# Optimization experiments

Hardware: AMD Instinct MI355X
Metric: run time of the kernel (lower is better)

Reference implementation:

```python
import jax, jax.numpy as jnp
import numpy as np

B, N, D_MODEL, HIDDEN, ACTION_BIN = 4096, 8, 1024, 2048, 256


def setup_inputs() -> dict:
    key = jax.random.key(0)
    k_x, k_w1, k_b1, k_w2, k_b2 = jax.random.split(key, 5)
    # per-action-dim MLP weights stacked along leading n axis
    s1 = 1.0 / np.sqrt(D_MODEL)
    s2 = 1.0 / np.sqrt(HIDDEN)
    return {
        "x": jax.random.normal(k_x, (B, N, D_MODEL), dtype=jnp.float32),
        "W1": jax.random.normal(k_w1, (N, D_MODEL, HIDDEN), dtype=jnp.float32) * s1,
        "b1": jax.random.normal(k_b1, (N, HIDDEN), dtype=jnp.float32) * s1,
        "W2": jax.random.normal(k_w2, (N, HIDDEN, ACTION_BIN), dtype=jnp.float32) * s2,
        "b2": jax.random.normal(k_b2, (N, ACTION_BIN), dtype=jnp.float32) * s2,
    }


def reference(x, W1, b1, W2, b2):
    # Original torch module loops over n slices, each with its own
    # Linear(d_model->hidden) -> ReLU -> Linear(hidden->action_bin).
    # Equivalent grouped/batched matmul over the n axis:
    x = x.astype(jnp.float32)
    h = jnp.einsum('bnd,ndh->bnh', x, W1) + b1[None, :, :]   # [b, n, hidden]
    h = jax.nn.relu(h)
    out = jnp.einsum('bnh,nha->bna', h, W2) + b2[None, :, :]  # [b, n, action_bin]
    return out
```

## Files before the change

### kernel.cpp

```cpp
#include <hip/hip_runtime.h>
#include <stdint.h>

#define BTOT   4096
#define NGRP   8
#define DMODEL 1024
#define HIDDEN 2048
#define ABIN   256

typedef short bf16x8 __attribute__((ext_vector_type(8)));
typedef float f32x4  __attribute__((ext_vector_type(4)));

__device__ __forceinline__ ushort f2bf(float f) {
    union { float f; uint32_t u; } v; v.f = f;
    return (ushort)((v.u + 0x7FFFu + ((v.u >> 16) & 1u)) >> 16);
}

__device__ __forceinline__ void gl_lds16(const ushort* g, ushort* l) {
    __builtin_amdgcn_global_load_lds(
        (const __attribute__((address_space(1))) uint32_t*)g,
        (__attribute__((address_space(3))) uint32_t*)l,
        16, 0, 0);
}

__global__ void transpose_w(const float* __restrict__ W, ushort* __restrict__ Wt,
                            int K, int N)
{
    __shared__ float tl[32][33];
    const int n  = blockIdx.y;
    const int nt = blockIdx.x % (N / 32);
    const int kt = blockIdx.x / (N / 32);
    const float* Wn  = W  + (size_t)n * K * N;
    ushort*      Wtn = Wt + (size_t)n * N * K;
    const int tx = threadIdx.x & 31, ty = threadIdx.x >> 5;
#pragma unroll
    for (int j = 0; j < 4; j++)
        tl[ty + 8 * j][tx] = Wn[(size_t)(kt * 32 + ty + 8 * j) * N + nt * 32 + tx];
    __syncthreads();
#pragma unroll
    for (int j = 0; j < 4; j++) {
        const int r = ty + 8 * j;
        Wtn[(size_t)(nt * 32 + r) * K + kt * 32 + tx] = f2bf(tl[tx][r]);
    }
}

__global__ void conv_x(const float* __restrict__ x, ushort* __restrict__ xb,
                       int CH, int cb)
{
    const int flat = blockIdx.x * 256 + threadIdx.x;
    const int d8 = flat & 127;
    const int rem = flat >> 7;
    const int n = rem & 7;
    const int r = rem >> 3;
    const float* src = x + ((size_t)(cb + r) * NGRP + n) * DMODEL + d8 * 8;
    float4 v0 = *(const float4*)(src);
    float4 v1 = *(const float4*)(src + 4);
    bf16x8 p;
    p[0] = (short)f2bf(v0.x); p[1] = (short)f2bf(v0.y);
    p[2] = (short)f2bf(v0.z); p[3] = (short)f2bf(v0.w);
    p[4] = (short)f2bf(v1.x); p[5] = (short)f2bf(v1.y);
    p[6] = (short)f2bf(v1.z); p[7] = (short)f2bf(v1.w);
    *(bf16x8*)(xb + ((size_t)n * CH + r) * DMODEL + d8 * 8) = p;
}

template<int MODE>
__global__ __launch_bounds__(256, 2)
void gemm_bt(const ushort* __restrict__ A, const ushort* __restrict__ Bt,
             const float* __restrict__ bias, void* __restrict__ outp,
             int CH, int cb)
{
    constexpr int K    = (MODE == 0) ? DMODEL : HIDDEN;
    constexpr int NDIM = (MODE == 0) ? HIDDEN : ABIN;
    constexpr int NT   = NDIM / 128;
    constexpr int BK   = 64;

    __shared__ __align__(16) ushort As[128 * BK];
    __shared__ __align__(16) ushort Bs[128 * BK];

    const int n  = blockIdx.y;
    const int mt = blockIdx.x / NT;
    const int nt = blockIdx.x % NT;

    const ushort* Ab = A  + ((size_t)n * CH   + mt * 128) * K;
    const ushort* Bb = Bt + ((size_t)n * NDIM + nt * 128) * K;

    const int t = threadIdx.x, l = t & 63, w = t >> 6;
    const int wr = w >> 1, wc = w & 1;
    const int lq = l >> 4, lr = l & 15;

    f32x4 acc[4][4];
#pragma unroll
    for (int i = 0; i < 4; i++)
#pragma unroll
        for (int j = 0; j < 4; j++) acc[i][j] = (f32x4){0.f, 0.f, 0.f, 0.f};

    for (int ki = 0; ki < K / BK; ++ki) {
        const ushort* Ak = Ab + ki * BK;
        const ushort* Bk = Bb + ki * BK;
        __syncthreads();
#pragma unroll
        for (int i = 0; i < 4; i++) {
            const int flat = t + 256 * i;
            const int row = flat >> 3, seg = flat & 7;
            gl_lds16(Ak + (size_t)row * K + seg * 8, (ushort*)As + flat * 8);
            gl_lds16(Bk + (size_t)row * K + seg * 8, (ushort*)Bs + flat * 8);
        }
        __syncthreads();

#pragma unroll
        for (int kk = 0; kk < 2; kk++) {
            bf16x8 af[4], bf[4];
#pragma unroll
            for (int m = 0; m < 4; m++)
                af[m] = *(const bf16x8*)&As[(wr * 64 + m * 16 + lr) * BK + kk * 32 + lq * 8];
#pragma unroll
            for (int nf = 0; nf < 4; nf++)
                bf[nf] = *(const bf16x8*)&Bs[(wc * 64 + nf * 16 + lr) * BK + kk * 32 + lq * 8];
#pragma unroll
            for (int m = 0; m < 4; m++)
#pragma unroll
                for (int nf = 0; nf < 4; nf++)
                    acc[m][nf] = __builtin_amdgcn_mfma_f32_16x16x32_bf16(af[m], bf[nf], acc[m][nf], 0, 0, 0);
        }
    }

#pragma unroll
    for (int nf = 0; nf < 4; nf++) {
        const int colg = nt * 128 + wc * 64 + nf * 16 + lr;
        const float bv = bias[(size_t)n * NDIM + colg];
#pragma unroll
        for (int m = 0; m < 4; m++) {
#pragma unroll
            for (int r = 0; r < 4; r++) {
                float vv = acc[m][nf][r] + bv;
                const int row = mt * 128 + wr * 64 + m * 16 + lq * 4 + r;
                if constexpr (MODE == 0) {
                    vv = fmaxf(vv, 0.f);
                    ((ushort*)outp)[((size_t)n * CH + row) * HIDDEN + colg] = f2bf(vv);
                } else {
                    ((float*)outp)[((size_t)(cb + row) * NGRP + n) * ABIN + colg] = vv;
                }
            }
        }
    }
}

extern "C" void kernel_launch(void* const* d_in, const int* in_sizes, int n_in,
                              void* d_out, int out_size, void* d_ws, size_t ws_size,
                              hipStream_t stream)
{
    const float* x  = (const float*)d_in[0];
    const float* W1 = (const float*)d_in[1];
    const float* b1 = (const float*)d_in[2];
    const float* W2 = (const float*)d_in[3];
    const float* b2 = (const float*)d_in[4];

    ushort* W1t = (ushort*)d_ws;
    ushort* W2t = W1t + (size_t)NGRP * HIDDEN * DMODEL;
    ushort* xb  = W2t + (size_t)NGRP * ABIN * HIDDEN;
    const size_t fixed = ((size_t)NGRP * HIDDEN * DMODEL + (size_t)NGRP * ABIN * HIDDEN) * 2;

    int CH = 4096;
    while (CH > 128 && fixed + (size_t)CH * (NGRP * (DMODEL + HIDDEN) * 2) > ws_size) CH >>= 1;
    ushort* h = xb + (size_t)NGRP * CH * DMODEL;

    {
        dim3 g1((DMODEL / 32) * (HIDDEN / 32), NGRP);
        transpose_w<<<g1, 256, 0, stream>>>(W1, W1t, DMODEL, HIDDEN);
        dim3 g2((HIDDEN / 32) * (ABIN / 32), NGRP);
        transpose_w<<<g2, 256, 0, stream>>>(W2, W2t, HIDDEN, ABIN);
    }

    for (int cb = 0; cb < BTOT; cb += CH) {
        conv_x<<<CH * 4, 256, 0, stream>>>(x, xb, CH, cb);
        dim3 g1((CH / 128) * (HIDDEN / 128), NGRP);
        gemm_bt<0><<<g1, 256, 0, stream>>>(xb, W1t, b1, h, CH, cb);
        dim3 g2((CH / 128) * (ABIN / 128), NGRP);
        gemm_bt<1><<<g2, 256, 0, stream>>>(h, W2t, b2, (float*)d_out, CH, cb);
    }
}
```

Baseline: 288.8 us.

## Replace first GEMM with 256x256-tile, 8-wave, double-buffered pipelined kernel

The first GEMM (x·W1 + bias + ReLU), which dominates the FLOPs, now runs in a dedicated kernel with 256x256 output tiles and 512 threads. It double-buffers 128KB of dynamic LDS, prefetching the next K-slab while MFMAs run on the current one. It adds an XOR-swizzled LDS layout to cut bank conflicts, a block-id swizzle for L2 locality, and s_setprio and sched_barrier hints around the MFMA bursts. The aim is to hide global-load latency and raise data reuse per tile, at the cost of heavy LDS use (one block per CU) and many explicit barriers and waitcnt steps.

```diff
diff --git a/kernel.cpp b/kernel.cpp
--- a/kernel.cpp
+++ b/kernel.cpp
@@ -62,17 +62,155 @@
     *(bf16x8*)(xb + ((size_t)n * CH + r) * DMODEL + d8 * 8) = p;
 }
 
-template<int MODE>
+#define REGN(buf,op,half,ks) (sm + ((((buf)*2+(op))*2+(half))*2+(ks))*4096)
+
+template<int MH>
+__device__ __forceinline__ void mma_q(f32x4 (&acc)[8][4], const bf16x8 (&af)[4],
+                                      const bf16x8 (&bv)[4])
+{
+#pragma unroll
+    for (int m4 = 0; m4 < 4; ++m4)
+#pragma unroll
+        for (int nf = 0; nf < 4; ++nf)
+            acc[MH * 4 + m4][nf] = __builtin_amdgcn_mfma_f32_16x16x32_bf16(
+                af[m4], bv[nf], acc[MH * 4 + m4][nf], 0, 0, 0);
+}
+
+__global__ __launch_bounds__(512, 2)
+void gemm8_1(const ushort* __restrict__ A, const ushort* __restrict__ Bt,
+             const float* __restrict__ bias, ushort* __restrict__ h, int CH)
+{
+    constexpr int K = DMODEL, NDIM = HIDDEN, KT = K / 64;
+    const int MT = CH >> 8, NT = NDIM >> 8;
+    extern __shared__ ushort sm[];
+
+    const int nwg = gridDim.x;
+    const int bid = blockIdx.x;
+    const int swz = (bid & 7) * (nwg >> 3) + (bid >> 3);
+    const int n   = swz / (MT * NT);
+    const int rem = swz - n * (MT * NT);
+    const int mt  = rem / NT;
+    const int nt  = rem - mt * NT;
+
+    const int tid = threadIdx.x;
+    const int l = tid & 63, wid = tid >> 6;
+    const int wr = wid >> 2, wc = wid & 3, wc2 = wc >> 1;
+    const int lq = l >> 4, lr = l & 15;
+
+    const ushort* Ab = A  + ((size_t)n * CH   + (size_t)mt * 256) * K;
+    const ushort* Bb = Bt + ((size_t)n * NDIM + (size_t)nt * 256) * K;
+
+    const int srow = tid >> 2;
+    const int sseg = (tid & 3) ^ (srow & 3);
+
+    auto stageA = [&](int b, int T, int ks) {
+        const size_t kofs = (size_t)T * 64 + ks * 32 + sseg * 8;
+        gl_lds16(Ab + (size_t)srow * K + kofs,         REGN(b, 0, 0, ks) + tid * 8);
+        gl_lds16(Ab + (size_t)(128 + srow) * K + kofs, REGN(b, 0, 1, ks) + tid * 8);
+    };
+    auto stageB = [&](int b, int T, int ks) {
+        const size_t kofs = (size_t)T * 64 + ks * 32 + sseg * 8;
+        gl_lds16(Bb + (size_t)srow * K + kofs,         REGN(b, 1, 0, ks) + tid * 8);
+        gl_lds16(Bb + (size_t)(128 + srow) * K + kofs, REGN(b, 1, 1, ks) + tid * 8);
+    };
+    auto ldA = [&](bf16x8 (&af)[4], int b, int kk, int mh) {
+#pragma unroll
+        for (int m4 = 0; m4 < 4; ++m4) {
+            const int rh = mh * 64 + m4 * 16 + lr;
+            af[m4] = *(const bf16x8*)(REGN(b, 0, wr, kk) + rh * 32 + (lq ^ (rh & 3)) * 8);
+        }
+    };
+    auto ldB = [&](bf16x8 (&bv)[4], int b, int kk) {
+#pragma unroll
+        for (int nf = 0; nf < 4; ++nf) {
+            const int rb = (wc & 1) * 64 + nf * 16 + lr;
+            bv[nf] = *(const bf16x8*)(REGN(b, 1, wc2, kk) + rb * 32 + (lq ^ (rb & 3)) * 8);
+        }
+    };
+
+    f32x4 acc[8][4];
+#pragma unroll
+    for (int i = 0; i < 8; ++i)
+#pragma unroll
+        for (int j = 0; j < 4; ++j) acc[i][j] = (f32x4){0.f, 0.f, 0.f, 0.f};
+
+    stageA(0, 0, 0); stageB(0, 0, 0); stageA(0, 0, 1); stageB(0, 0, 1);
+    asm volatile("s_waitcnt vmcnt(4)" ::: "memory");
+    __builtin_amdgcn_s_barrier();
+
+    bf16x8 af[4], bv[4];
+    for (int g = 0; g < KT; ++g) {
+        const int c = g & 1;
+        const bool ns = (g + 1 < KT);
+
+        ldA(af, c, 0, 0); ldB(bv, c, 0);
+        if (ns) stageA(c ^ 1, g + 1, 0);
+        __builtin_amdgcn_s_barrier();
+        asm volatile("s_waitcnt lgkmcnt(0)" ::: "memory");
+        __builtin_amdgcn_sched_barrier(0);
+        __builtin_amdgcn_s_setprio(1);
+        mma_q<0>(acc, af, bv);
+        __builtin_amdgcn_s_setprio(0);
+        __builtin_amdgcn_s_barrier();
+
+        ldA(af, c, 0, 1);
+        if (ns) stageB(c ^ 1, g + 1, 0);
+        __builtin_amdgcn_s_barrier();
+        asm volatile("s_waitcnt lgkmcnt(0)" ::: "memory");
+        __builtin_amdgcn_sched_barrier(0);
+        __builtin_amdgcn_s_setprio(1);
+        mma_q<1>(acc, af, bv);
+        __builtin_amdgcn_s_setprio(0);
+        if (ns) asm volatile("s_waitcnt vmcnt(4)" ::: "memory");
+        else    asm volatile("s_waitcnt vmcnt(0)" ::: "memory");
+        __builtin_amdgcn_s_barrier();
+
+        ldA(af, c, 1, 0); ldB(bv, c, 1);
+        if (ns) stageA(c ^ 1, g + 1, 1);
+        __builtin_amdgcn_s_barrier();
+        asm volatile("s_waitcnt lgkmcnt(0)" ::: "memory");
+        __builtin_amdgcn_sched_barrier(0);
+        __builtin_amdgcn_s_setprio(1);
+        mma_q<0>(acc, af, bv);
+        __builtin_amdgcn_s_setprio(0);
+        __builtin_amdgcn_s_barrier();
+
+        ldA(af, c, 1, 1);
+        if (ns) stageB(c ^ 1, g + 1, 1);
+        __builtin_amdgcn_s_barrier();
+        asm volatile("s_waitcnt lgkmcnt(0)" ::: "memory");
+        __builtin_amdgcn_sched_barrier(0);
+        __builtin_amdgcn_s_setprio(1);
+        mma_q<1>(acc, af, bv);
+        __builtin_amdgcn_s_setprio(0);
+        if (ns) asm volatile("s_waitcnt vmcnt(4)" ::: "memory");
+        __builtin_amdgcn_s_barrier();
+    }
+
+    __builtin_amdgcn_sched_barrier(0);
+
+#pragma unroll
+    for (int nf = 0; nf < 4; ++nf) {
+        const int col = nt * 256 + wc * 64 + nf * 16 + lr;
+        const float bvv = bias[(size_t)n * NDIM + col];
+#pragma unroll
+        for (int m = 0; m < 8; ++m) {
+#pragma unroll
+            for (int r = 0; r < 4; ++r) {
+                const int row = mt * 256 + wr * 128 + m * 16 + lq * 4 + r;
+                float vv = fmaxf(acc[m][nf][r] + bvv, 0.f);
+                h[((size_t)n * CH + row) * HIDDEN + col] = f2bf(vv);
+            }
+        }
+    }
+}
+
 __global__ __launch_bounds__(256, 2)
-void gemm_bt(const ushort* __restrict__ A, const ushort* __restrict__ Bt,
-             const float* __restrict__ bias, void* __restrict__ outp,
-             int CH, int cb)
-{
-    constexpr int K    = (MODE == 0) ? DMODEL : HIDDEN;
-    constexpr int NDIM = (MODE == 0) ? HIDDEN : ABIN;
-    constexpr int NT   = NDIM / 128;
-    constexpr int BK   = 64;
-
+void gemm2(const ushort* __restrict__ A, const ushort* __restrict__ Bt,
+           const float* __restrict__ bias, float* __restrict__ outp,
+           int CH, int cb)
+{
+    constexpr int K = HIDDEN, NDIM = ABIN, NT = NDIM / 128, BK = 64;
     __shared__ __align__(16) ushort As[128 * BK];
     __shared__ __align__(16) ushort Bs[128 * BK];
 
@@ -131,14 +269,8 @@
         for (int m = 0; m < 4; m++) {
 #pragma unroll
             for (int r = 0; r < 4; r++) {
-                float vv = acc[m][nf][r] + bv;
                 const int row = mt * 128 + wr * 64 + m * 16 + lq * 4 + r;
-                if constexpr (MODE == 0) {
-                    vv = fmaxf(vv, 0.f);
-                    ((ushort*)outp)[((size_t)n * CH + row) * HIDDEN + colg] = f2bf(vv);
-                } else {
-                    ((float*)outp)[((size_t)(cb + row) * NGRP + n) * ABIN + colg] = vv;
-                }
+                outp[((size_t)(cb + row) * NGRP + n) * ABIN + colg] = acc[m][nf][r] + bv;
             }
         }
     }
@@ -154,13 +286,16 @@
     const float* W2 = (const float*)d_in[3];
     const float* b2 = (const float*)d_in[4];
 
+    hipFuncSetAttribute((const void*)gemm8_1,
+                        hipFuncAttributeMaxDynamicSharedMemorySize, 131072);
+
     ushort* W1t = (ushort*)d_ws;
     ushort* W2t = W1t + (size_t)NGRP * HIDDEN * DMODEL;
     ushort* xb  = W2t + (size_t)NGRP * ABIN * HIDDEN;
     const size_t fixed = ((size_t)NGRP * HIDDEN * DMODEL + (size_t)NGRP * ABIN * HIDDEN) * 2;
 
     int CH = 4096;
-    while (CH > 128 && fixed + (size_t)CH * (NGRP * (DMODEL + HIDDEN) * 2) > ws_size) CH >>= 1;
+    while (CH > 256 && fixed + (size_t)CH * (NGRP * (DMODEL + HIDDEN) * 2) > ws_size) CH >>= 1;
     ushort* h = xb + (size_t)NGRP * CH * DMODEL;
 
     {
@@ -172,9 +307,9 @@
 
     for (int cb = 0; cb < BTOT; cb += CH) {
         conv_x<<<CH * 4, 256, 0, stream>>>(x, xb, CH, cb);
-        dim3 g1((CH / 128) * (HIDDEN / 128), NGRP);
-        gemm_bt<0><<<g1, 256, 0, stream>>>(xb, W1t, b1, h, CH, cb);
+        const int g1 = NGRP * (CH / 256) * (HIDDEN / 256);
+        gemm8_1<<<g1, 512, 131072, stream>>>(xb, W1t, b1, h, CH);
         dim3 g2((CH / 128) * (ABIN / 128), NGRP);
-        gemm_bt<1><<<g2, 256, 0, stream>>>(h, W2t, b2, (float*)d_out, CH, cb);
-    }
-}
+        gemm2<<<g2, 256, 0, stream>>>(h, W2t, b2, (float*)d_out, CH, cb);
+    }
+}
```

After: 292.9 us. No clear change (+1.4%).
